# Kernel optimization log

Hardware: AMD Instinct MI355X
Metric: run time of the kernel (lower is better)

Reference implementation:

```python
import jax, jax.numpy as jnp
import numpy as np
from jax import lax

K_NEIGH = 20
BN_EPS = 1e-5


def conv2d(x, w, b, pad):
    # x: [B,C,H,W], w: [O,I,kh,kw]
    y = lax.conv_general_dilated(x, w, (1, 1), [(pad, pad), (pad, pad)],
                                 dimension_numbers=('NCHW', 'OIHW', 'NCHW'))
    return y + b[None, :, None, None]


def bn_train(h, gamma, beta):
    # h: [B,N,K,C]; BatchNorm1d in train mode: stats over (B,N,K) per channel
    mean = jnp.mean(h, axis=(0, 1, 2), keepdims=True)
    var = jnp.mean(jnp.square(h - mean), axis=(0, 1, 2), keepdims=True)
    return gamma * (h - mean) * lax.rsqrt(var + BN_EPS) + beta


def edge_conv(F1, w1, b1, g1, bt1, w2, b2, g2, bt2):
    # F1: [B,N,F] with F=1
    B, N, Fd = F1.shape
    sq = jnp.sum(F1 * F1, axis=-1)                               # [B,N]
    dist = sq[:, :, None] + sq[:, None, :] - 2.0 * jnp.einsum('bnf,bmf->bnm', F1, F1)
    idx = jnp.argsort(dist, axis=-1)[:, :, 1:K_NEIGH + 1]        # [B,N,K]
    knn = jax.vmap(lambda xb, ib: xb[ib])(F1, idx)               # [B,N,K,F]
    x1 = jnp.broadcast_to(F1[:, :, None, :], (B, N, K_NEIGH, Fd))
    x_in = jnp.concatenate([x1, knn - x1], axis=-1)              # [B,N,K,2F]
    h = jnp.einsum('bnkc,oc->bnko', x_in, w1) + b1               # 1x1 conv1d
    h = jax.nn.relu(bn_train(h, g1, bt1))
    o = jnp.einsum('bnkc,oc->bnko', h, w2) + b2
    o = jax.nn.relu(bn_train(o, g2, bt2))
    return jnp.max(o, axis=2)                                    # [B,N,an]


def pixel_shuffle(x, r):
    B, C, H, W = x.shape
    x = x.reshape(B, C // (r * r), r, r, H, W)
    x = x.transpose(0, 1, 4, 2, 5, 3)
    return x.reshape(B, C // (r * r), H * r, W * r)


def setup_inputs() -> dict:
    key = jax.random.key(0)
    ks = jax.random.split(key, 8)
    B, H, W = 4, 64, 64
    inp = {
        'x':   jax.random.normal(ks[0], (B, 1, H, W), jnp.float32),
        'c1w': jax.random.normal(ks[1], (64, 1, 5, 5), jnp.float32) * 0.1,
        'c1b': jnp.zeros((64,), jnp.float32),
        'c2w': jax.random.normal(ks[2], (32, 64, 3, 3), jnp.float32) * 0.05,
        'c2b': jnp.zeros((32,), jnp.float32),
        'c3w': jax.random.normal(ks[3], (16, 32, 3, 3), jnp.float32) * 0.05,
        'c3b': jnp.zeros((16,), jnp.float32),
        'c4w': jax.random.normal(ks[4], (1, 16, 3, 3), jnp.float32) * 0.05,
        'c4b': jnp.zeros((1,), jnp.float32),
        'ew1': jax.random.normal(ks[5], (3, 16, 2), jnp.float32) * 0.5,
        'eb1': jnp.zeros((3, 16), jnp.float32),
        'eg1': jnp.ones((3, 16), jnp.float32),
        'ebt1': jnp.zeros((3, 16), jnp.float32),
        'ew2': jax.random.normal(ks[6], (3, 1, 16), jnp.float32) * 0.25,
        'eb2': jnp.zeros((3, 1), jnp.float32),
        'eg2': jnp.ones((3, 1), jnp.float32),
        'ebt2': jnp.zeros((3, 1), jnp.float32),
    }
    return inp


def reference(x, c1w, c1b, c2w, c2b, c3w, c3b, c4w, c4b,
              ew1, eb1, eg1, ebt1, ew2, eb2, eg2, ebt2):
    h = jnp.tanh(conv2d(x, c1w, c1b, 2))
    h = jnp.tanh(conv2d(h, c2w, c2b, 1))
    h = jnp.tanh(conv2d(h, c3w, c3b, 1))
    h = conv2d(h, c4w, c4b, 1)                     # [B,1,H,W]
    B, C, H, W = h.shape
    F1 = h.reshape(B, C, H * W).transpose(0, 2, 1)  # [B,N,1]
    branches = [h]
    for i in range(3):
        o = edge_conv(F1, ew1[i], eb1[i], eg1[i], ebt1[i],
                      ew2[i], eb2[i], eg2[i], ebt2[i])  # [B,N,1]
        branches.append(o.transpose(0, 2, 1).reshape(B, C, H, W))
    p = jnp.concatenate(branches, axis=1)          # [B,4,H,W]
    return jax.nn.sigmoid(pixel_shuffle(p, 2))     # [B,1,2H,2W]
```

## Files before the change

kernel.cpp:

```cpp
#include <hip/hip_runtime.h>
#include <math.h>

#define NPIX 4096
#define KN 20
#define MTOT 327680.0

__device__ inline unsigned long long shflx64(unsigned long long v, int m) {
  unsigned lo = (unsigned)v, hi = (unsigned)(v >> 32);
  lo = __shfl_xor(lo, m, 64);
  hi = __shfl_xor(hi, m, 64);
  return (((unsigned long long)hi) << 32) | lo;
}

__global__ __launch_bounds__(512) void conv12_k(const float* __restrict__ x,
    const float* __restrict__ c1w, const float* __restrict__ c1b,
    const float* __restrict__ c2w, const float* __restrict__ c2b,
    float* __restrict__ part12) {
  __shared__ float sx[506];
  __shared__ float sc1[5472];
  const int tid = threadIdx.x;
  const int b = blockIdx.x, tile = blockIdx.y, z = blockIdx.z;
  const int th = (tile >> 2) << 4, tw = (tile & 3) << 4;

  for (int i = tid; i < 484; i += 512) {
    int r = i / 22, c = i - r*22;
    int gr = th - 3 + r, gc = tw - 3 + c;
    sx[r*23 + c] = (gr>=0 && gr<64 && gc>=0 && gc<64) ? x[b*NPIX + (gr<<6) + gc] : 0.f;
  }
  __syncthreads();
  for (int idx = tid; idx < 5184; idx += 512) {
    int co = idx / 324, rem = idx - co*324;
    int i = rem / 18, j = rem - i*18;
    int gy = th - 1 + i, gx = tw - 1 + j;
    bool inb = (gy>=0 && gy<64 && gx>=0 && gx<64);
    int cg = (z << 4) + co;
    float acc = c1b[cg];
#pragma unroll
    for (int di=0; di<5; di++)
#pragma unroll
      for (int dj=0; dj<5; dj++)
        acc = fmaf(sx[(i+di)*23 + j+dj], c1w[cg*25 + di*5 + dj], acc);
    sc1[co*342 + i*19 + j] = inb ? tanhf(acc) : 0.f;
  }
  __syncthreads();
  {
    const int l = tid & 63;
    const int w = __builtin_amdgcn_readfirstlane(tid >> 6);
    int row0 = (l >> 4) << 2;
    int col  = l & 15;
    int co0 = w << 2;
    float acc[16];
#pragma unroll
    for (int p=0;p<4;p++)
#pragma unroll
      for (int q=0;q<4;q++)
        acc[p*4+q] = (z == 0) ? c2b[co0+q] : 0.f;
#pragma unroll 2
    for (int ci = 0; ci < 16; ci++) {
      const float* sp = sc1 + ci*342;
      float vb[6][3];
#pragma unroll
      for (int r=0;r<6;r++)
#pragma unroll
        for (int dj=0;dj<3;dj++)
          vb[r][dj] = sp[(row0+r)*19 + col + dj];
      int cin = (z << 4) + ci;
#pragma unroll
      for (int q=0;q<4;q++) {
        const float* wq = c2w + ((size_t)(co0+q)*64 + cin)*9;
#pragma unroll
        for (int p=0;p<4;p++) {
          float a = acc[p*4+q];
#pragma unroll
          for (int di=0;di<3;di++)
#pragma unroll
            for (int dj=0;dj<3;dj++)
              a = fmaf(vb[p+di][dj], wq[di*3+dj], a);
          acc[p*4+q] = a;
        }
      }
    }
#pragma unroll
    for (int q=0;q<4;q++)
#pragma unroll
      for (int p=0;p<4;p++)
        part12[(((size_t)(z*4 + b)*32 + co0+q) << 12)
               + ((th+row0+p)<<6) + tw + col] = acc[p*4+q];
  }
}

__global__ __launch_bounds__(512) void conv34_k(const float* __restrict__ part12,
    const float* __restrict__ c3w, const float* __restrict__ c3b,
    const float* __restrict__ c4w, const float* __restrict__ c4b,
    float* __restrict__ fbuf) {
  __shared__ float sc2[4992];
  __shared__ float sc3[2080];
  const int tid = threadIdx.x;
  const int b = blockIdx.x, tile = blockIdx.y;
  const int th = (tile >> 3) << 3, tw = (tile & 7) << 3;
  const int px = tid & 127;
  const int coutg = __builtin_amdgcn_readfirstlane(tid >> 7);

  for (int i = tid; i < 4608; i += 512) {
    int cin = i / 144, rem = i - cin*144;
    int rr = rem / 12, cc = rem - rr*12;
    int gr = th - 2 + rr, gc = tw - 2 + cc;
    float v = 0.f;
    if (gr>=0 && gr<64 && gc>=0 && gc<64) {
      size_t idx = (((size_t)b*32 + cin) << 12) + (gr<<6) + gc;
      v = tanhf(part12[idx] + part12[idx + 524288] +
                part12[idx + 1048576] + part12[idx + 1572864]);
    }
    sc2[cin*156 + rr*13 + cc] = v;
  }
  __syncthreads();
  if (px < 100) {
    int pi = px / 10, pj = px - pi*10;
    int co0 = coutg << 2;
    float a0 = c3b[co0+0], a1 = c3b[co0+1], a2 = c3b[co0+2], a3 = c3b[co0+3];
    for (int cin = 0; cin < 32; cin++) {
      const float* sp = sc2 + cin*156;
      float v[9];
#pragma unroll
      for (int di=0;di<3;di++)
#pragma unroll
        for (int dj=0;dj<3;dj++)
          v[di*3+dj] = sp[(pi+di)*13 + pj+dj];
      const float* wc = c3w + cin*9;
      const float* w0p = wc + (size_t)(co0+0)*288;
      const float* w1p = wc + (size_t)(co0+1)*288;
      const float* w2p = wc + (size_t)(co0+2)*288;
      const float* w3p = wc + (size_t)(co0+3)*288;
#pragma unroll
      for (int t=0;t<9;t++) {
        a0 = fmaf(v[t], w0p[t], a0);
        a1 = fmaf(v[t], w1p[t], a1);
        a2 = fmaf(v[t], w2p[t], a2);
        a3 = fmaf(v[t], w3p[t], a3);
      }
    }
    int gy = th - 1 + pi, gx = tw - 1 + pj;
    bool inb = (gy>=0 && gy<64 && gx>=0 && gx<64);
    sc3[(co0+0)*130 + pi*13 + pj] = inb ? tanhf(a0) : 0.f;
    sc3[(co0+1)*130 + pi*13 + pj] = inb ? tanhf(a1) : 0.f;
    sc3[(co0+2)*130 + pi*13 + pj] = inb ? tanhf(a2) : 0.f;
    sc3[(co0+3)*130 + pi*13 + pj] = inb ? tanhf(a3) : 0.f;
  }
  __syncthreads();
  if (tid < 64) {
    int py = tid >> 3, qx = tid & 7;
    float acc4 = c4b[0];
    for (int cin = 0; cin < 16; cin++) {
#pragma unroll
      for (int di=0;di<3;di++)
#pragma unroll
        for (int dj=0;dj<3;dj++)
          acc4 = fmaf(sc3[cin*130 + (py+di)*13 + qx+dj], c4w[cin*9 + di*3+dj], acc4);
    }
    fbuf[b*NPIX + ((th+py)<<6) + (tw+qx)] = acc4;
  }
}

__global__ __launch_bounds__(1024) void sort2_k(const float* __restrict__ f,
    float* __restrict__ sval, int* __restrict__ sidx) {
  int b = blockIdx.x;
  int tid = threadIdx.x;
  int l = tid & 63, w = tid >> 6;
  __shared__ unsigned long long Ab[NPIX];
  __shared__ unsigned long long Bb[NPIX];
  const float* fb = f + b*NPIX;
  unsigned long long key[4];
#pragma unroll
  for (int r=0;r<4;r++) {
    unsigned e = (w<<8) + (r<<6) + l;
    float v = fb[e];
    unsigned u = __float_as_uint(v);
    u ^= (u >> 31) ? 0xFFFFFFFFu : 0x80000000u;
    key[r] = (((unsigned long long)u) << 32) | e;
  }
  for (unsigned k = 2; k <= 256; k <<= 1) {
    for (unsigned j = k >> 1; j > 0; j >>= 1) {
      if (j >= 64) {
        unsigned rj = j >> 6;
#pragma unroll
        for (int r=0;r<4;r++) {
          int pr = r ^ (int)rj;
          if (pr > r) {
            unsigned e = (w<<8)+((unsigned)r<<6)+l;
            bool up = ((e & k & 255u) == 0);
            unsigned long long a = key[r], c = key[pr];
            bool sw = up ? (c < a) : (c > a);
            if (sw) { key[r] = c; key[pr] = a; }
          }
        }
      } else {
#pragma unroll
        for (int r=0;r<4;r++) {
          unsigned e = (w<<8)+((unsigned)r<<6)+l;
          unsigned long long a = key[r];
          unsigned long long p = shflx64(a, (int)j);
          bool up = ((e & k & 255u) == 0);
          bool keepmin = ((e & j) == 0) == up;
          key[r] = (keepmin ? (p < a) : (p > a)) ? p : a;
        }
      }
    }
  }
#pragma unroll
  for (int r=0;r<4;r++) Ab[(w<<8)+(r<<6)+l] = key[r];
  __syncthreads();
  unsigned long long* src = Ab;
  unsigned long long* dst = Bb;
  for (int lg = 8; lg <= 11; lg++) {
    const int L = 1 << lg;
    int p0 = tid << 2;
    int ri = p0 >> lg;
    int base = (ri ^ 1) << lg;
    int mbase = ((ri >> 1) << (lg + 1)) + (p0 & (L - 1));
    unsigned long long kk[4];
    int lo[4], hi[4];
#pragma unroll
    for (int r=0;r<4;r++) { kk[r] = src[p0 + r]; lo[r] = 0; hi[r] = L; }
    for (int s = 0; s <= lg; s++) {
#pragma unroll
      for (int r=0;r<4;r++) {
        if (lo[r] < hi[r]) {
          int mid = (lo[r] + hi[r]) >> 1;
          if (src[base + mid] < kk[r]) lo[r] = mid + 1; else hi[r] = mid;
        }
      }
    }
#pragma unroll
    for (int r=0;r<4;r++) dst[mbase + r + lo[r]] = kk[r];
    __syncthreads();
    unsigned long long* t = src; src = dst; dst = t;
  }
#pragma unroll
  for (int r=0;r<4;r++) {
    int p = (tid << 2) + r;
    unsigned long long kk = src[p];
    unsigned u = (unsigned)(kk >> 32);
    u ^= (u >> 31) ? 0x80000000u : 0xFFFFFFFFu;
    sval[b*NPIX + p] = __uint_as_float(u);
    sidx[b*NPIX + p] = (int)(kk & 0xFFFFFFFFu);
  }
}

__global__ __launch_bounds__(512) void knn4_k(const float* __restrict__ f,
    const float* __restrict__ sval, const int* __restrict__ sidx,
    float* __restrict__ dout, double* __restrict__ part1) {
  const int tid = threadIdx.x, blk = blockIdx.x;
  const int l = tid & 63, w = tid >> 6;
  const int bq = blk >> 7;
  const float* svb = sval + (bq << 12);
  const int*   sib = sidx + (bq << 12);
  const float* fB  = f + (bq << 12);
  double a0=0, a1=0, a2=0, a3=0, a4=0;
  unsigned long long kk[4];
  float fnp[4];
  int   sp[4];
#pragma unroll
  for (int p=0;p<4;p++) {
    int s = ((blk & 127) << 5) + (w << 2) + p;
    sp[p] = s;
    float fn = svb[s]; fnp[p] = fn;
    int start = s - 32;
    if (start < 0) start = 0;
    if (start > NPIX - 64) start = NPIX - 64;
    int q = start + l;
    float fm = svb[q];
    int   m  = sib[q];
    float sqn = __fmul_rn(fn, fn);
    float pr  = __fmul_rn(fn, fm);
    float dist = __fsub_rn(__fadd_rn(sqn, __fmul_rn(fm, fm)), __fmul_rn(2.0f, pr));
    unsigned u = __float_as_uint(dist);
    u ^= (u >> 31) ? 0xFFFFFFFFu : 0x80000000u;
    kk[p] = (((unsigned long long)u) << 32) | (unsigned)m;
  }
#pragma unroll
  for (int k = 2; k <= 64; k <<= 1)
#pragma unroll
    for (int j = k >> 1; j > 0; j >>= 1) {
#pragma unroll
      for (int p=0;p<4;p++) {
        unsigned long long pp = shflx64(kk[p], j);
        bool up = ((l & k) == 0);
        bool keepmin = ((l & j) == 0) == up;
        kk[p] = (keepmin ? (pp < kk[p]) : (pp > kk[p])) ? pp : kk[p];
      }
    }
#pragma unroll
  for (int p=0;p<4;p++) {
    int mr = (int)(kk[p] & 0xFFFFFFFFu);
    float fn = fnp[p];
    float d = __fsub_rn(fB[mr], fn);
    int n = sib[sp[p]];
    if (l >= 1 && l <= 20)
      dout[(size_t)((bq<<12) + n)*KN + (l-1)] = d;
    float dm = (l >= 1 && l <= 20) ? d : 0.f;
    a2 += (double)dm;
    a3 += (double)dm * (double)dm;
    a4 += (double)fn * (double)dm;
    if (l == 0) { a0 += (double)fn; a1 += (double)fn * (double)fn; }
  }
  double v[5] = {a0, a1, a2, a3, a4};
#pragma unroll
  for (int qi=0; qi<5; qi++)
    for (int off=32; off>0; off>>=1) v[qi] += __shfl_down(v[qi], off, 64);
  __shared__ double sred[8][5];
  if (l == 0)
#pragma unroll
    for (int qi=0; qi<5; qi++) sred[w][qi] = v[qi];
  __syncthreads();
  if (tid == 0) {
#pragma unroll
    for (int qi=0; qi<5; qi++) {
      double s = 0.0;
#pragma unroll
      for (int ww=0; ww<8; ww++) s += sred[ww][qi];
      part1[blk*5 + qi] = s;
    }
  }
}

__global__ __launch_bounds__(64) void branch_k(const float* __restrict__ f,
    const float* __restrict__ dw, const double* __restrict__ part1,
    const float* __restrict__ ew1, const float* __restrict__ eb1,
    const float* __restrict__ eg1, const float* __restrict__ ebt1,
    const float* __restrict__ ew2, const float* __restrict__ eb2,
    float* __restrict__ maxo, float* __restrict__ mino,
    double* __restrict__ part2) {
  const int l = threadIdx.x;
  const int blk = blockIdx.x, br = blockIdx.y;
  double a[5] = {0,0,0,0,0};
  for (int b2 = l; b2 < 512; b2 += 64)
#pragma unroll
    for (int q=0;q<5;q++) a[q] += part1[b2*5+q];
#pragma unroll
  for (int q=0;q<5;q++)
    for (int off=32; off>0; off>>=1) a[q] += __shfl_down(a[q], off, 64);
#pragma unroll
  for (int q=0;q<5;q++) a[q] = __shfl(a[q], 0, 64);
  double Ef = a[0]/16384.0, Eff = a[1]/16384.0;
  double Ed = a[2]/MTOT, Edd = a[3]/MTOT, Efd = a[4]/MTOT;
  double Vf = Eff - Ef*Ef, Vd = Edd - Ed*Ed, Cfd = Efd - Ef*Ed;
  float sA[16], sB[16], sC[16], sW[16];
#pragma unroll
  for (int c=0;c<16;c++) {
    int idx = br*16 + c;
    double w0 = (double)ew1[idx*2+0], w1 = (double)ew1[idx*2+1];
    double b1 = (double)eb1[idx];
    double m1 = w0*Ef + w1*Ed + b1;
    double v1 = w0*w0*Vf + 2.0*w0*w1*Cfd + w1*w1*Vd;
    double r1 = 1.0 / sqrt(v1 + 1e-5);
    double g = (double)eg1[idx];
    sA[c] = (float)(g*r1*w0);
    sB[c] = (float)(g*r1*w1);
    sC[c] = (float)(g*r1*(b1 - m1) + (double)ebt1[idx]);
    sW[c] = ew2[idx];
  }
  int row = (blk << 6) + l;
  float fv = f[row];
  const float* dd = dw + (size_t)row*KN;
  float b2v = eb2[br];
  float P[16];
#pragma unroll
  for (int c=0;c<16;c++) P[c] = fmaf(sA[c], fv, sC[c]);
  float mx = -INFINITY, mn = INFINITY;
  double s = 0.0, s2 = 0.0;
  for (int k=0;k<KN;k++) {
    float d = dd[k];
    float t = b2v;
#pragma unroll
    for (int c=0;c<16;c++)
      t = fmaf(sW[c], fmaxf(fmaf(sB[c], d, P[c]), 0.f), t);
    mx = fmaxf(mx, t);
    mn = fminf(mn, t);
    double td = (double)t;
    s += td; s2 += td*td;
  }
  maxo[br*16384 + row] = mx;
  mino[br*16384 + row] = mn;
#pragma unroll
  for (int off=32; off>0; off>>=1) {
    s  += __shfl_down(s, off, 64);
    s2 += __shfl_down(s2, off, 64);
  }
  if (l == 0) {
    part2[(br*256 + blk)*2 + 0] = s;
    part2[(br*256 + blk)*2 + 1] = s2;
  }
}

__global__ __launch_bounds__(256) void out_k(const float* __restrict__ f,
    const float* __restrict__ maxo, const float* __restrict__ mino,
    const double* __restrict__ part2,
    const float* __restrict__ eg2, const float* __restrict__ ebt2,
    float* __restrict__ out) {
  __shared__ float c2c[3][2];
  const int tid = threadIdx.x, blk = blockIdx.x;
  const int l = tid & 63, w = tid >> 6;
  if (w < 3) {
    int br = w;
    double s = 0.0, s2 = 0.0;
#pragma unroll
    for (int i=0;i<4;i++) {
      int bb = l + (i << 6);
      s  += part2[(br*256 + bb)*2 + 0];
      s2 += part2[(br*256 + bb)*2 + 1];
    }
#pragma unroll
    for (int off=32; off>0; off>>=1) {
      s  += __shfl_down(s, off, 64);
      s2 += __shfl_down(s2, off, 64);
    }
    if (l == 0) {
      double mean = s / MTOT;
      double var = s2 / MTOT - mean*mean;
      double r2 = 1.0 / sqrt(var + 1e-5);
      double sc = (double)eg2[br] * r2;
      c2c[br][0] = (float)sc;
      c2c[br][1] = (float)((double)ebt2[br] - sc*mean);
    }
  }
  __syncthreads();
  int tg = (blk << 8) + tid;
  int bo = tg >> 14;
  int y = (tg >> 7) & 127, xx = tg & 127;
  int n = ((y>>1)<<6) + (xx>>1);
  int ch = ((y&1)<<1) + (xx&1);
  float v;
  if (ch == 0) {
    v = f[bo*NPIX + n];
  } else {
    int br = ch - 1;
    float sc = c2c[br][0], sh = c2c[br][1];
    float base = (sc >= 0.f) ? maxo[br*16384 + bo*NPIX + n]
                             : mino[br*16384 + bo*NPIX + n];
    v = fmaxf(fmaf(sc, base, sh), 0.f);
  }
  out[tg] = 1.f / (1.f + expf(-v));
}

extern "C" void kernel_launch(void* const* d_in, const int* in_sizes, int n_in,
                              void* d_out, int out_size, void* d_ws, size_t ws_size,
                              hipStream_t stream) {
  (void)in_sizes; (void)n_in; (void)out_size; (void)ws_size;
  const float* x    = (const float*)d_in[0];
  const float* c1w  = (const float*)d_in[1];
  const float* c1b  = (const float*)d_in[2];
  const float* c2w  = (const float*)d_in[3];
  const float* c2b  = (const float*)d_in[4];
  const float* c3w  = (const float*)d_in[5];
  const float* c3b  = (const float*)d_in[6];
  const float* c4w  = (const float*)d_in[7];
  const float* c4b  = (const float*)d_in[8];
  const float* ew1  = (const float*)d_in[9];
  const float* eb1  = (const float*)d_in[10];
  const float* eg1  = (const float*)d_in[11];
  const float* ebt1 = (const float*)d_in[12];
  const float* ew2  = (const float*)d_in[13];
  const float* eb2  = (const float*)d_in[14];
  const float* eg2  = (const float*)d_in[15];
  const float* ebt2 = (const float*)d_in[16];
  float* out = (float*)d_out;
  float* ws  = (float*)d_ws;

  float*  part12 = ws;
  float*  fbuf  = ws + 2097152;
  float*  dw    = ws + 2113536;
  float*  sval  = ws + 2441216;
  int*    sidx  = (int*)(ws + 2457600);
  float*  maxo  = ws + 2473984;
  float*  mino  = ws + 2523136;
  double* part1 = (double*)(ws + 2572288);
  double* part2 = (double*)(ws + 2577408);

  conv12_k<<<dim3(4,16,4), 512, 0, stream>>>(x, c1w, c1b, c2w, c2b, part12);
  conv34_k<<<dim3(4,64), 512, 0, stream>>>(part12, c3w, c3b, c4w, c4b, fbuf);
  sort2_k<<<4, 1024, 0, stream>>>(fbuf, sval, sidx);
  knn4_k<<<512, 512, 0, stream>>>(fbuf, sval, sidx, dw, part1);
  branch_k<<<dim3(256,3), 64, 0, stream>>>(fbuf, dw, part1,
      ew1, eb1, eg1, ebt1, ew2, eb2, maxo, mino, part2);
  out_k<<<256, 256, 0, stream>>>(fbuf, maxo, mino, part2, eg2, ebt2, out);
}
```

Baseline: 104.3 us.

## Fuse sort and kNN into one kernel with redundant per-block full bitonic sort

```diff
diff --git a/kernel.cpp b/kernel.cpp
--- a/kernel.cpp
+++ b/kernel.cpp
@@ -10,6 +10,21 @@
   lo = __shfl_xor(lo, m, 64);
   hi = __shfl_xor(hi, m, 64);
   return (((unsigned long long)hi) << 32) | lo;
+}
+
+template<int RJ>
+__device__ inline void regstage8(unsigned long long (&key)[8], unsigned k, int l, int w) {
+#pragma unroll
+  for (int r = 0; r < 8; r++) {
+    int pr = r ^ RJ;
+    if (pr > r) {
+      unsigned e = ((unsigned)w << 9) + ((unsigned)r << 6) + (unsigned)l;
+      bool up = ((e & k) == 0);
+      unsigned long long a = key[r], c = key[pr];
+      bool sw = up ? (c < a) : (c > a);
+      if (sw) { key[r] = c; key[pr] = a; }
+    }
+  }
 }
 
 __global__ __launch_bounds__(512) void conv12_k(const float* __restrict__ x,
@@ -161,153 +176,123 @@
   }
 }
 
-__global__ __launch_bounds__(1024) void sort2_k(const float* __restrict__ f,
-    float* __restrict__ sval, int* __restrict__ sidx) {
-  int b = blockIdx.x;
-  int tid = threadIdx.x;
-  int l = tid & 63, w = tid >> 6;
-  __shared__ unsigned long long Ab[NPIX];
-  __shared__ unsigned long long Bb[NPIX];
-  const float* fb = f + b*NPIX;
-  unsigned long long key[4];
-#pragma unroll
-  for (int r=0;r<4;r++) {
-    unsigned e = (w<<8) + (r<<6) + l;
+__global__ __launch_bounds__(512) void sortknn_k(const float* __restrict__ f,
+    float* __restrict__ dout, double* __restrict__ part1) {
+  __shared__ unsigned long long keys[NPIX];
+  __shared__ double sred[8][5];
+  const int tid = threadIdx.x, blk = blockIdx.x;
+  const int l = tid & 63, w = tid >> 6;
+  const int bq = blk >> 6;
+  const float* fb = f + (bq << 12);
+
+  unsigned long long key[8];
+#pragma unroll
+  for (int r=0;r<8;r++) {
+    unsigned e = ((unsigned)w<<9) + ((unsigned)r<<6) + (unsigned)l;
     float v = fb[e];
     unsigned u = __float_as_uint(v);
     u ^= (u >> 31) ? 0xFFFFFFFFu : 0x80000000u;
     key[r] = (((unsigned long long)u) << 32) | e;
   }
-  for (unsigned k = 2; k <= 256; k <<= 1) {
+  for (unsigned k = 2; k <= 4096; k <<= 1) {
     for (unsigned j = k >> 1; j > 0; j >>= 1) {
-      if (j >= 64) {
-        unsigned rj = j >> 6;
-#pragma unroll
-        for (int r=0;r<4;r++) {
-          int pr = r ^ (int)rj;
-          if (pr > r) {
-            unsigned e = (w<<8)+((unsigned)r<<6)+l;
-            bool up = ((e & k & 255u) == 0);
-            unsigned long long a = key[r], c = key[pr];
-            bool sw = up ? (c < a) : (c > a);
-            if (sw) { key[r] = c; key[pr] = a; }
-          }
+      if (j >= 512) {
+        __syncthreads();
+#pragma unroll
+        for (int r=0;r<8;r++) keys[((unsigned)w<<9)+((unsigned)r<<6)+l] = key[r];
+        __syncthreads();
+#pragma unroll
+        for (int r=0;r<8;r++) {
+          unsigned e = ((unsigned)w<<9)+((unsigned)r<<6)+(unsigned)l;
+          unsigned long long p = keys[e ^ j];
+          bool up = ((e & k) == 0);
+          bool keepmin = ((e & j) == 0) == up;
+          key[r] = (keepmin ? (p < key[r]) : (p > key[r])) ? p : key[r];
+        }
+      } else if (j >= 64) {
+        switch (j >> 6) {
+          case 1: regstage8<1>(key, k, l, w); break;
+          case 2: regstage8<2>(key, k, l, w); break;
+          default: regstage8<4>(key, k, l, w); break;
         }
       } else {
 #pragma unroll
-        for (int r=0;r<4;r++) {
-          unsigned e = (w<<8)+((unsigned)r<<6)+l;
-          unsigned long long a = key[r];
-          unsigned long long p = shflx64(a, (int)j);
-          bool up = ((e & k & 255u) == 0);
+        for (int r=0;r<8;r++) {
+          unsigned e = ((unsigned)w<<9)+((unsigned)r<<6)+(unsigned)l;
+          unsigned long long p = shflx64(key[r], (int)j);
+          bool up = ((e & k) == 0);
           bool keepmin = ((e & j) == 0) == up;
-          key[r] = (keepmin ? (p < a) : (p > a)) ? p : a;
+          key[r] = (keepmin ? (p < key[r]) : (p > key[r])) ? p : key[r];
         }
       }
     }
   }
-#pragma unroll
-  for (int r=0;r<4;r++) Ab[(w<<8)+(r<<6)+l] = key[r];
-  __syncthreads();
-  unsigned long long* src = Ab;
-  unsigned long long* dst = Bb;
-  for (int lg = 8; lg <= 11; lg++) {
-    const int L = 1 << lg;
-    int p0 = tid << 2;
-    int ri = p0 >> lg;
-    int base = (ri ^ 1) << lg;
-    int mbase = ((ri >> 1) << (lg + 1)) + (p0 & (L - 1));
+  __syncthreads();
+#pragma unroll
+  for (int r=0;r<8;r++) keys[((unsigned)w<<9)+((unsigned)r<<6)+l] = key[r];
+  __syncthreads();
+
+  const int pbase = (blk & 63) << 6;
+  double a0=0, a1=0, a2=0, a3=0, a4=0;
+  for (int half = 0; half < 2; half++) {
     unsigned long long kk[4];
-    int lo[4], hi[4];
-#pragma unroll
-    for (int r=0;r<4;r++) { kk[r] = src[p0 + r]; lo[r] = 0; hi[r] = L; }
-    for (int s = 0; s <= lg; s++) {
-#pragma unroll
-      for (int r=0;r<4;r++) {
-        if (lo[r] < hi[r]) {
-          int mid = (lo[r] + hi[r]) >> 1;
-          if (src[base + mid] < kk[r]) lo[r] = mid + 1; else hi[r] = mid;
+    float fnp[4];
+    int   sp[4];
+#pragma unroll
+    for (int p=0;p<4;p++) {
+      int s = pbase + (w << 3) + (half << 2) + p;
+      sp[p] = s;
+      unsigned long long ks = keys[s];
+      unsigned uf = (unsigned)(ks >> 32);
+      uf ^= (uf >> 31) ? 0x80000000u : 0xFFFFFFFFu;
+      float fn = __uint_as_float(uf);
+      fnp[p] = fn;
+      int start = s - 32;
+      if (start < 0) start = 0;
+      if (start > NPIX - 64) start = NPIX - 64;
+      unsigned long long kc = keys[start + l];
+      unsigned um = (unsigned)(kc >> 32);
+      um ^= (um >> 31) ? 0x80000000u : 0xFFFFFFFFu;
+      float fm = __uint_as_float(um);
+      int m = (int)(kc & 0xFFFFFFFFu);
+      float sqn = __fmul_rn(fn, fn);
+      float pr  = __fmul_rn(fn, fm);
+      float dist = __fsub_rn(__fadd_rn(sqn, __fmul_rn(fm, fm)), __fmul_rn(2.0f, pr));
+      unsigned u = __float_as_uint(dist);
+      u ^= (u >> 31) ? 0xFFFFFFFFu : 0x80000000u;
+      kk[p] = (((unsigned long long)u) << 32) | (unsigned)m;
+    }
+#pragma unroll
+    for (int k = 2; k <= 64; k <<= 1)
+#pragma unroll
+      for (int j = k >> 1; j > 0; j >>= 1) {
+#pragma unroll
+        for (int p=0;p<4;p++) {
+          unsigned long long pp = shflx64(kk[p], j);
+          bool up = ((l & k) == 0);
+          bool keepmin = ((l & j) == 0) == up;
+          kk[p] = (keepmin ? (pp < kk[p]) : (pp > kk[p])) ? pp : kk[p];
         }
       }
-    }
-#pragma unroll
-    for (int r=0;r<4;r++) dst[mbase + r + lo[r]] = kk[r];
-    __syncthreads();
-    unsigned long long* t = src; src = dst; dst = t;
-  }
-#pragma unroll
-  for (int r=0;r<4;r++) {
-    int p = (tid << 2) + r;
-    unsigned long long kk = src[p];
-    unsigned u = (unsigned)(kk >> 32);
-    u ^= (u >> 31) ? 0x80000000u : 0xFFFFFFFFu;
-    sval[b*NPIX + p] = __uint_as_float(u);
-    sidx[b*NPIX + p] = (int)(kk & 0xFFFFFFFFu);
-  }
-}
-
-__global__ __launch_bounds__(512) void knn4_k(const float* __restrict__ f,
-    const float* __restrict__ sval, const int* __restrict__ sidx,
-    float* __restrict__ dout, double* __restrict__ part1) {
-  const int tid = threadIdx.x, blk = blockIdx.x;
-  const int l = tid & 63, w = tid >> 6;
-  const int bq = blk >> 7;
-  const float* svb = sval + (bq << 12);
-  const int*   sib = sidx + (bq << 12);
-  const float* fB  = f + (bq << 12);
-  double a0=0, a1=0, a2=0, a3=0, a4=0;
-  unsigned long long kk[4];
-  float fnp[4];
-  int   sp[4];
-#pragma unroll
-  for (int p=0;p<4;p++) {
-    int s = ((blk & 127) << 5) + (w << 2) + p;
-    sp[p] = s;
-    float fn = svb[s]; fnp[p] = fn;
-    int start = s - 32;
-    if (start < 0) start = 0;
-    if (start > NPIX - 64) start = NPIX - 64;
-    int q = start + l;
-    float fm = svb[q];
-    int   m  = sib[q];
-    float sqn = __fmul_rn(fn, fn);
-    float pr  = __fmul_rn(fn, fm);
-    float dist = __fsub_rn(__fadd_rn(sqn, __fmul_rn(fm, fm)), __fmul_rn(2.0f, pr));
-    unsigned u = __float_as_uint(dist);
-    u ^= (u >> 31) ? 0xFFFFFFFFu : 0x80000000u;
-    kk[p] = (((unsigned long long)u) << 32) | (unsigned)m;
-  }
-#pragma unroll
-  for (int k = 2; k <= 64; k <<= 1)
-#pragma unroll
-    for (int j = k >> 1; j > 0; j >>= 1) {
-#pragma unroll
-      for (int p=0;p<4;p++) {
-        unsigned long long pp = shflx64(kk[p], j);
-        bool up = ((l & k) == 0);
-        bool keepmin = ((l & j) == 0) == up;
-        kk[p] = (keepmin ? (pp < kk[p]) : (pp > kk[p])) ? pp : kk[p];
-      }
-    }
-#pragma unroll
-  for (int p=0;p<4;p++) {
-    int mr = (int)(kk[p] & 0xFFFFFFFFu);
-    float fn = fnp[p];
-    float d = __fsub_rn(fB[mr], fn);
-    int n = sib[sp[p]];
-    if (l >= 1 && l <= 20)
-      dout[(size_t)((bq<<12) + n)*KN + (l-1)] = d;
-    float dm = (l >= 1 && l <= 20) ? d : 0.f;
-    a2 += (double)dm;
-    a3 += (double)dm * (double)dm;
-    a4 += (double)fn * (double)dm;
-    if (l == 0) { a0 += (double)fn; a1 += (double)fn * (double)fn; }
+#pragma unroll
+    for (int p=0;p<4;p++) {
+      int mr = (int)(kk[p] & 0xFFFFFFFFu);
+      float fn = fnp[p];
+      float d = __fsub_rn(fb[mr], fn);
+      int n = (int)(keys[sp[p]] & 0xFFFFFFFFu);
+      if (l >= 1 && l <= 20)
+        dout[(size_t)((bq<<12) + n)*KN + (l-1)] = d;
+      float dm = (l >= 1 && l <= 20) ? d : 0.f;
+      a2 += (double)dm;
+      a3 += (double)dm * (double)dm;
+      a4 += (double)fn * (double)dm;
+      if (l == 0) { a0 += (double)fn; a1 += (double)fn * (double)fn; }
+    }
   }
   double v[5] = {a0, a1, a2, a3, a4};
 #pragma unroll
   for (int qi=0; qi<5; qi++)
     for (int off=32; off>0; off>>=1) v[qi] += __shfl_down(v[qi], off, 64);
-  __shared__ double sred[8][5];
   if (l == 0)
 #pragma unroll
     for (int qi=0; qi<5; qi++) sred[w][qi] = v[qi];
@@ -333,7 +318,7 @@
   const int l = threadIdx.x;
   const int blk = blockIdx.x, br = blockIdx.y;
   double a[5] = {0,0,0,0,0};
-  for (int b2 = l; b2 < 512; b2 += 64)
+  for (int b2 = l; b2 < 256; b2 += 64)
 #pragma unroll
     for (int q=0;q<5;q++) a[q] += part1[b2*5+q];
 #pragma unroll
@@ -469,17 +454,14 @@
   float*  part12 = ws;
   float*  fbuf  = ws + 2097152;
   float*  dw    = ws + 2113536;
-  float*  sval  = ws + 2441216;
-  int*    sidx  = (int*)(ws + 2457600);
-  float*  maxo  = ws + 2473984;
-  float*  mino  = ws + 2523136;
-  double* part1 = (double*)(ws + 2572288);
-  double* part2 = (double*)(ws + 2577408);
+  float*  maxo  = ws + 2441216;
+  float*  mino  = ws + 2490368;
+  double* part1 = (double*)(ws + 2539520);
+  double* part2 = (double*)(ws + 2542080);
 
   conv12_k<<<dim3(4,16,4), 512, 0, stream>>>(x, c1w, c1b, c2w, c2b, part12);
   conv34_k<<<dim3(4,64), 512, 0, stream>>>(part12, c3w, c3b, c4w, c4b, fbuf);
-  sort2_k<<<4, 1024, 0, stream>>>(fbuf, sval, sidx);
-  knn4_k<<<512, 512, 0, stream>>>(fbuf, sval, sidx, dw, part1);
+  sortknn_k<<<256, 512, 0, stream>>>(fbuf, dw, part1);
   branch_k<<<dim3(256,3), 64, 0, stream>>>(fbuf, dw, part1,
       ew1, eb1, eg1, ebt1, ew2, eb2, maxo, mino, part2);
   out_k<<<256, 256, 0, stream>>>(fbuf, maxo, mino, part2, eg2, ebt2, out);
```

New measurement: 133.4 us. +27.9%, slower.
